# Kernel optimization log

Hardware: AMD Instinct MI355X
Metric: run time of the kernel (lower is better)

The kernel has to match this reference:

```python
import jax, jax.numpy as jnp
import numpy as np

B, S, D, H, L, FF, V, NB, G, C = 8, 1024, 256, 8, 2, 1024, 32000, 20000, 12, 4
DH = D // H


def _layer_norm(x, g, b, eps=1e-5):
    m = x.mean(-1, keepdims=True)
    v = ((x - m) ** 2).mean(-1, keepdims=True)
    return (x - m) / jnp.sqrt(v + eps) * g + b


def setup_inputs() -> dict:
    key = jax.random.key(0)
    ks = jax.random.split(key, 32)
    w = lambda k, shape, s=0.05: (jax.random.normal(k, shape, dtype=jnp.float32) * s)
    inp = {
        'input_ids': jax.random.randint(ks[0], (B, S), 0, V),
        'ngram_ids': jax.random.randint(ks[1], (V, G), 0, NB),
        'tfidf_scores': jax.random.uniform(ks[2], (V,), dtype=jnp.float32),
        'emb': jax.random.uniform(ks[3], (V, D), minval=-0.1, maxval=0.1, dtype=jnp.float32).at[0].set(0.0),  # padding_idx=0 row zeroed
        'pos_enc': jax.random.normal(ks[4], (1, S, D), dtype=jnp.float32) * 0.01,
        'bucket_emb': jax.random.uniform(ks[5], (NB, D), minval=-0.05, maxval=0.05, dtype=jnp.float32),
        'Wq': w(ks[6], (L, D, D)), 'bq': jnp.zeros((L, D)),
        'Wk': w(ks[7], (L, D, D)), 'bk': jnp.zeros((L, D)),
        'Wv': w(ks[8], (L, D, D)), 'bv': jnp.zeros((L, D)),
        'Wo': w(ks[9], (L, D, D)), 'bo': jnp.zeros((L, D)),
        'g1': jnp.ones((L, D)), 'be1': jnp.zeros((L, D)),
        'g2': jnp.ones((L, D)), 'be2': jnp.zeros((L, D)),
        'W1': w(ks[10], (L, D, FF)), 'b1': jnp.zeros((L, FF)),
        'W2': w(ks[11], (L, FF, D)), 'b2': jnp.zeros((L, D)),
        'alpha': jnp.full((L,), 0.1, dtype=jnp.float32),
        'gf': jnp.ones((D,)), 'bf': jnp.zeros((D,)),
        'Wc': jax.random.uniform(ks[12], (D, C), minval=-0.1, maxval=0.1, dtype=jnp.float32),
        'bc': jnp.zeros((C,)),
    }
    return inp


def reference(input_ids, ngram_ids, tfidf_scores, emb, pos_enc, bucket_emb,
              Wq, bq, Wk, bk, Wv, bv, Wo, bo, g1, be1, g2, be2,
              W1, b1, W2, b2, alpha, gf, bf, Wc, bc):
    pad_mask = input_ids == 0                      # (B,S) key padding mask
    x = emb[input_ids] + pos_enc[:, :S]            # (B,S,D)
    # char n-gram embedding: masked mean over n-gram buckets
    tok_ng = ngram_ids[jnp.clip(input_ids, 0, ngram_ids.shape[0] - 1)]   # (B,S,G)
    e_ng = bucket_emb[tok_ng]                       # (B,S,G,D)
    m = (tok_ng != 0)[..., None].astype(x.dtype)
    x = x + (e_ng * m).sum(axis=2) / jnp.clip(m.sum(axis=2), 1.0, None)
    # TF-IDF bias per key position
    bias_base = tfidf_scores[jnp.clip(input_ids, 0, tfidf_scores.shape[0] - 1)]  # (B,S)
    scale = DH ** -0.5
    for l in range(L):
        x2 = _layer_norm(x, g1[l], be1[l])
        Q = (x2 @ Wq[l] + bq[l]).reshape(B, S, H, DH).transpose(0, 2, 1, 3)
        K = (x2 @ Wk[l] + bk[l]).reshape(B, S, H, DH).transpose(0, 2, 1, 3)
        Vv = (x2 @ Wv[l] + bv[l]).reshape(B, S, H, DH).transpose(0, 2, 1, 3)
        scores = jnp.einsum('bhqd,bhkd->bhqk', Q, K) * scale
        scores = scores + (bias_base * alpha[l])[:, None, None, :]
        scores = jnp.where(pad_mask[:, None, None, :], -jnp.inf, scores)
        attn = jax.nn.softmax(scores, axis=-1)
        out = jnp.einsum('bhqk,bhkd->bhqd', attn, Vv).transpose(0, 2, 1, 3).reshape(B, S, D)
        x = x + (out @ Wo[l] + bo[l])
        x2 = _layer_norm(x, g2[l], be2[l])
        x = x + (jax.nn.relu(x2 @ W1[l] + b1[l]) @ W2[l] + b2[l])
    x = _layer_norm(x, gf, bf)
    return x[:, 0] @ Wc + bc                        # CLS pooling -> (B,4)
```

## Files before the change

### kernel.cpp

```cpp
#include <hip/hip_runtime.h>
#include <hip/hip_bf16.h>
#include <math.h>

#define TOK 8192
#define DIM 256
#define SEQ 1024
#define NH 8
#define FFD 1024
#define NL 2
#define VOCAB 32000
#define QKSTRIDE 2097152

typedef short bf16x8 __attribute__((ext_vector_type(8)));
typedef float f32x4 __attribute__((ext_vector_type(4)));

__device__ __forceinline__ ushort f2bf(float f) {
  union { float f; uint32_t u; } v; v.f = f;
  uint32_t r = v.u + 0x7FFFu + ((v.u >> 16) & 1u);
  return (ushort)(r >> 16);
}

__device__ __forceinline__ float bf2f(ushort u) {
  union { uint32_t u; float f; } v; v.u = (uint32_t)u << 16; return v.f;
}

__device__ __forceinline__ float exp2_n(float x) {
  float r; asm("v_exp_f32 %0, %1" : "=v"(r) : "v"(x)); return r;
}

__device__ __forceinline__ uint32_t cvtpk(float lo, float hi) {
  uint32_t r; asm("v_cvt_pk_bf16_f32 %0, %1, %2" : "=v"(r) : "v"(lo), "v"(hi));
  return r;
}

__device__ __forceinline__ void gload_lds16(const ushort* gp, ushort* lp) {
  __builtin_amdgcn_global_load_lds(
      (const __attribute__((address_space(1))) void*)gp,
      (__attribute__((address_space(3))) void*)lp, 16, 0, 0);
}

__global__ __launch_bounds__(256) void embed_ln_kernel(
    const int* __restrict__ ids, const int* __restrict__ ngram_ids,
    const float* __restrict__ tfidf, const float* __restrict__ emb,
    const float* __restrict__ pos, const float* __restrict__ bucket,
    const float* __restrict__ alpha, const float* __restrict__ g1,
    const float* __restrict__ be1,
    float* __restrict__ x, ushort* __restrict__ x2b, float* __restrict__ bm2)
{
  __shared__ int ngs[12];
  __shared__ float red[2][4];
  const int t = blockIdx.x;
  const int id = ids[t];
  int idc = id; if (idc < 0) idc = 0; if (idc > VOCAB-1) idc = VOCAB-1;
  if (threadIdx.x < 12) ngs[threadIdx.x] = ngram_ids[idc*12 + threadIdx.x];
  if (threadIdx.x == 0) {
    const float tf = tfidf[idc];
    const bool msk = (id == 0);
    const float l2e = 1.4426950408889634f;
    bm2[t]       = msk ? -1e30f : tf * alpha[0] * l2e;
    bm2[TOK + t] = msk ? -1e30f : tf * alpha[1] * l2e;
  }
  __syncthreads();
  const int d = threadIdx.x;
  const int s = t & (SEQ - 1);
  float v = emb[(size_t)id*DIM + d] + pos[s*DIM + d];
  float sum = 0.f; int cnt = 0;
  #pragma unroll
  for (int g = 0; g < 12; ++g) {
    const int ng = ngs[g];
    if (ng != 0) { sum += bucket[(size_t)ng*DIM + d]; cnt++; }
  }
  v += sum / fmaxf((float)cnt, 1.0f);
  x[(size_t)t*DIM + d] = v;
  const int wave = d >> 6, lane = d & 63;
  float sm = v;
  #pragma unroll
  for (int o = 32; o >= 1; o >>= 1) sm += __shfl_xor(sm, o);
  if (lane == 0) red[0][wave] = sm;
  __syncthreads();
  const float mean = (red[0][0]+red[0][1]+red[0][2]+red[0][3]) * (1.f/256.f);
  const float dv = v - mean;
  float q = dv * dv;
  #pragma unroll
  for (int o = 32; o >= 1; o >>= 1) q += __shfl_xor(q, o);
  if (lane == 0) red[1][wave] = q;
  __syncthreads();
  const float var = (red[1][0]+red[1][1]+red[1][2]+red[1][3]) * (1.f/256.f);
  const float rs = rsqrtf(var + 1e-5f);
  x2b[(size_t)t*DIM + d] = f2bf(dv*rs*g1[d] + be1[d]);
}

__global__ __launch_bounds__(256) void ln_bf16(
    const float* __restrict__ x, const float* __restrict__ g,
    const float* __restrict__ b, ushort* __restrict__ y)
{
  const int wave = threadIdx.x >> 6, lane = threadIdx.x & 63;
  const int row = blockIdx.x * 4 + wave;
  const float* xr = x + (size_t)row * DIM;
  float4 v = *reinterpret_cast<const float4*>(xr + lane*4);
  float s = v.x + v.y + v.z + v.w;
  #pragma unroll
  for (int o = 32; o >= 1; o >>= 1) s += __shfl_xor(s, o);
  const float mean = s * (1.f/256.f);
  const float dx0 = v.x-mean, dx1 = v.y-mean, dx2 = v.z-mean, dx3 = v.w-mean;
  float q = dx0*dx0 + dx1*dx1 + dx2*dx2 + dx3*dx3;
  #pragma unroll
  for (int o = 32; o >= 1; o >>= 1) q += __shfl_xor(q, o);
  const float rs = rsqrtf(q * (1.f/256.f) + 1e-5f);
  float4 gv = *reinterpret_cast<const float4*>(g + lane*4);
  float4 bv = *reinterpret_cast<const float4*>(b + lane*4);
  ushort4 o4;
  o4.x = f2bf(dx0*rs*gv.x + bv.x);
  o4.y = f2bf(dx1*rs*gv.y + bv.y);
  o4.z = f2bf(dx2*rs*gv.z + bv.z);
  o4.w = f2bf(dx3*rs*gv.w + bv.w);
  *reinterpret_cast<ushort4*>(y + (size_t)row*DIM + lane*4) = o4;
}

struct TDesc { const float* src; ushort* dst; int K; int N; };
struct TDescs { TDesc d[12]; };

__global__ __launch_bounds__(256) void transpose_conv(TDescs descs)
{
  const TDesc t = descs.d[blockIdx.z];
  const int k0 = blockIdx.x * 32, n0 = blockIdx.y * 32;
  if (k0 >= t.K || n0 >= t.N) return;
  __shared__ float tile[32][33];
  const int r = threadIdx.x >> 5, cc = threadIdx.x & 31;
  #pragma unroll
  for (int i = 0; i < 4; ++i)
    tile[r + i*8][cc] = t.src[(size_t)(k0 + r + i*8)*t.N + n0 + cc];
  __syncthreads();
  #pragma unroll
  for (int i = 0; i < 4; ++i)
    t.dst[(size_t)(n0 + r + i*8)*t.K + k0 + cc] = f2bf(tile[cc][r + i*8]);
}

template<int KDIM, int NDIM, int MODE>
__global__ __launch_bounds__(256) void gemm_mfma(
    const ushort* __restrict__ A, const ushort* __restrict__ Bw,
    const float* __restrict__ bias0, const float* __restrict__ bias1,
    const float* __restrict__ bias2, void* __restrict__ Cout,
    ushort* __restrict__ vtb)
{
  __shared__ ushort Al[3][64*32];
  __shared__ ushort Bl[3][128*32];
  const int bm = blockIdx.y * 64, bn = blockIdx.x * 128;
  const int tid = threadIdx.x, w = tid >> 6, lane = tid & 63;
  const int g = lane >> 4, c = lane & 15;
  const int lrow = lane >> 2, lc8 = (lane & 3) << 3;
  const f32x4 fzero = {0.f, 0.f, 0.f, 0.f};
  f32x4 acc[4][2];
  #pragma unroll
  for (int m = 0; m < 4; ++m) { acc[m][0] = fzero; acc[m][1] = fzero; }

#define STAGE(buf, k0)                                                         \
  {                                                                            \
    _Pragma("unroll")                                                          \
    for (int ch = w; ch < 12; ch += 4) {                                       \
      if (ch < 4)                                                              \
        gload_lds16(A + (size_t)(bm + ch*16 + lrow)*KDIM + (k0) + lc8,         \
                    &Al[buf][ch*512]);                                         \
      else                                                                     \
        gload_lds16(Bw + (size_t)(bn + (ch-4)*16 + lrow)*KDIM + (k0) + lc8,    \
                    &Bl[buf][(ch-4)*512]);                                     \
    }                                                                          \
  }

#define COMPUTE(buf)                                                           \
  {                                                                            \
    bf16x8 af[4], bfr[2];                                                      \
    _Pragma("unroll")                                                          \
    for (int m = 0; m < 4; ++m)                                                \
      af[m] = *(const bf16x8*)&Al[buf][(m*16 + c)*32 + g*8];                   \
    _Pragma("unroll")                                                          \
    for (int n = 0; n < 2; ++n)                                                \
      bfr[n] = *(const bf16x8*)&Bl[buf][(w*32 + n*16 + c)*32 + g*8];           \
    _Pragma("unroll")                                                          \
    for (int m = 0; m < 4; ++m)                                                \
      _Pragma("unroll")                                                        \
      for (int n = 0; n < 2; ++n)                                              \
        acc[m][n] = __builtin_amdgcn_mfma_f32_16x16x32_bf16(af[m], bfr[n], acc[m][n], 0, 0, 0); \
  }

  STAGE(0, 0);
  STAGE(1, 32);
  STAGE(2, 64);
  int buf = 0;
  for (int k0 = 0; k0 + 64 < KDIM; k0 += 32) {
    asm volatile("s_waitcnt vmcnt(6)" ::: "memory");
    __builtin_amdgcn_s_barrier();
    COMPUTE(buf);
    asm volatile("s_waitcnt lgkmcnt(0)" ::: "memory");
    __builtin_amdgcn_s_barrier();
    if (k0 + 96 < KDIM) STAGE(buf, k0 + 96);
    buf = (buf == 2) ? 0 : buf + 1;
  }
  asm volatile("s_waitcnt vmcnt(3)" ::: "memory");
  __builtin_amdgcn_s_barrier();
  COMPUTE(buf);
  buf = (buf == 2) ? 0 : buf + 1;
  asm volatile("s_waitcnt vmcnt(0)" ::: "memory");
  __builtin_amdgcn_s_barrier();
  COMPUTE(buf);
#undef STAGE
#undef COMPUTE

  #pragma unroll
  for (int m = 0; m < 4; ++m) {
    const int row0 = bm + m*16 + g*4;
    #pragma unroll
    for (int n = 0; n < 2; ++n) {
      const int col = bn + w*32 + n*16 + c;
      if (MODE == 1) {
        const float bb = bias0[col];
        #pragma unroll
        for (int r = 0; r < 4; ++r) {
          const float vv = fmaxf(acc[m][n][r] + bb, 0.f);
          const float other = __shfl_xor(vv, 1);
          if ((c & 1) == 0) {
            const uint32_t word = (uint32_t)f2bf(vv) | ((uint32_t)f2bf(other) << 16);
            *(uint32_t*)((ushort*)Cout + (size_t)(row0 + r)*NDIM + col) = word;
          }
        }
      } else if (MODE == 4) {
        const int b_ = row0 >> 10, s = row0 & (SEQ - 1);
        const int hd = col & 255;
        const int hh = hd >> 5, d = hd & 31;
        const float bb = (col < 256) ? bias0[hd] : bias1[hd];
        ushort* dst = ((col < 256) ? (ushort*)Cout : vtb)
                    + (((size_t)(b_*NH + hh)*SEQ + s) << 5) + d;
        #pragma unroll
        for (int r = 0; r < 4; ++r) {
          const float vv = acc[m][n][r] + bb;
          const float other = __shfl_xor(vv, 1);
          if ((c & 1) == 0) {
            const uint32_t word = (uint32_t)f2bf(vv) | ((uint32_t)f2bf(other) << 16);
            *(uint32_t*)(dst + (r << 5)) = word;
          }
        }
      } else {
        const int b_ = row0 >> 10, s = row0 & (SEQ - 1);
        if (col < 512) {
          const int hd = col & 255;
          const int hh = hd >> 5, d = hd & 31;
          const float bb = (col < 256) ? bias0[hd] : bias1[hd];
          ushort* dst = (ushort*)Cout + (col < 256 ? 0 : QKSTRIDE)
                      + (((size_t)(b_*NH + hh)*SEQ + s) << 5) + d;
          #pragma unroll
          for (int r = 0; r < 4; ++r) {
            const float vv = acc[m][n][r] + bb;
            const float other = __shfl_xor(vv, 1);
            if ((c & 1) == 0) {
              const uint32_t word = (uint32_t)f2bf(vv) | ((uint32_t)f2bf(other) << 16);
              *(uint32_t*)(dst + (r << 5)) = word;
            }
          }
        } else {
          const int hd = col - 512;
          const int hh = hd >> 5, d = hd & 31;
          const float bb = bias2[hd];
          const int sg = s >> 5, a = (s & 31) >> 2;
          const int pbase = (a & 3)*8 + (a >> 2)*4;
          ushort4 w4;
          w4.x = f2bf(acc[m][n][0] + bb);
          w4.y = f2bf(acc[m][n][1] + bb);
          w4.z = f2bf(acc[m][n][2] + bb);
          w4.w = f2bf(acc[m][n][3] + bb);
          *(ushort4*)(vtb + (((size_t)((b_*NH + hh)*32 + sg)*32 + d) << 5) + pbase) = w4;
        }
      }
    }
  }
}

template<int KDIM>
__global__ __launch_bounds__(256) void gemm64_acc(
    const ushort* __restrict__ A, const ushort* __restrict__ Bw,
    const float* __restrict__ bias, float* __restrict__ C)
{
  __shared__ ushort Al[3][64*32];
  __shared__ ushort Bl[3][64*32];
  const int bm = blockIdx.y * 64, bn = blockIdx.x * 64;
  const int tid = threadIdx.x, w = tid >> 6, lane = tid & 63;
  const int wm = w >> 1, wn = w & 1;
  const int g = lane >> 4, c = lane & 15;
  const int lrow = tid >> 2, lc8 = (tid & 3) << 3;
  const f32x4 fzero = {0.f, 0.f, 0.f, 0.f};
  f32x4 acc[2][2];
  acc[0][0] = fzero; acc[0][1] = fzero; acc[1][0] = fzero; acc[1][1] = fzero;

#define STAGE64(buf, k0)                                                       \
  {                                                                            \
    gload_lds16(A  + (size_t)(bm + lrow)*KDIM + (k0) + lc8,                    \
                &Al[buf][lrow*32 + lc8]);                                      \
    gload_lds16(Bw + (size_t)(bn + lrow)*KDIM + (k0) + lc8,                    \
                &Bl[buf][lrow*32 + lc8]);                                      \
  }

#define COMPUTE64(buf)                                                         \
  {                                                                            \
    bf16x8 af[2], bfr[2];                                                      \
    _Pragma("unroll")                                                          \
    for (int m = 0; m < 2; ++m)                                                \
      af[m] = *(const bf16x8*)&Al[buf][(wm*32 + m*16 + c)*32 + g*8];           \
    _Pragma("unroll")                                                          \
    for (int n = 0; n < 2; ++n)                                                \
      bfr[n] = *(const bf16x8*)&Bl[buf][(wn*32 + n*16 + c)*32 + g*8];          \
    _Pragma("unroll")                                                          \
    for (int m = 0; m < 2; ++m)                                                \
      _Pragma("unroll")                                                        \
      for (int n = 0; n < 2; ++n)                                              \
        acc[m][n] = __builtin_amdgcn_mfma_f32_16x16x32_bf16(af[m], bfr[n], acc[m][n], 0, 0, 0); \
  }

  STAGE64(0, 0);
  STAGE64(1, 32);
  STAGE64(2, 64);
  int buf = 0;
  for (int k0 = 0; k0 + 64 < KDIM; k0 += 32) {
    asm volatile("s_waitcnt vmcnt(4)" ::: "memory");
    __builtin_amdgcn_s_barrier();
    COMPUTE64(buf);
    asm volatile("s_waitcnt lgkmcnt(0)" ::: "memory");
    __builtin_amdgcn_s_barrier();
    if (k0 + 96 < KDIM) STAGE64(buf, k0 + 96);
    buf = (buf == 2) ? 0 : buf + 1;
  }
  asm volatile("s_waitcnt vmcnt(2)" ::: "memory");
  __builtin_amdgcn_s_barrier();
  COMPUTE64(buf);
  buf = (buf == 2) ? 0 : buf + 1;
  asm volatile("s_waitcnt vmcnt(0)" ::: "memory");
  __builtin_amdgcn_s_barrier();
  COMPUTE64(buf);
#undef STAGE64
#undef COMPUTE64

  #pragma unroll
  for (int m = 0; m < 2; ++m) {
    const int row0 = bm + wm*32 + m*16 + g*4;
    #pragma unroll
    for (int n = 0; n < 2; ++n) {
      const int col = bn + wn*32 + n*16 + c;
      const float bb = bias[col];
      #pragma unroll
      for (int r = 0; r < 4; ++r)
        C[(size_t)(row0 + r)*DIM + col] += acc[m][n][r] + bb;
    }
  }
}

__global__ __launch_bounds__(256) void attn_mfma(
    const ushort* __restrict__ qh, const ushort* __restrict__ kh,
    const ushort* __restrict__ vph, const float* __restrict__ bm2l,
    ushort* __restrict__ O)
{
  const int bid = blockIdx.x;
  const int lin = ((bid & 7) << 8) + (bid >> 3);
  const int tid = threadIdx.x, w = tid >> 6, lane = tid & 63;
  const int qw = lin & 31, h = (lin >> 5) & 7, b = lin >> 8;
  const int qb = qw << 5;
  const float scale2 = 0.17677669529663687f * 1.4426950408889634f;
  const int g = lane >> 4, c = lane & 15;
  const f32x4 fzero = {0.f, 0.f, 0.f, 0.f};
  const size_t bh = (size_t)(b*NH + h);

  const bf16x8 qf0 = *(const bf16x8*)(qh + ((bh*SEQ + qb + c)      << 5) + g*8);
  const bf16x8 qf1 = *(const bf16x8*)(qh + ((bh*SEQ + qb + 16 + c) << 5) + g*8);
  const ushort* kbase = kh  + ((bh*SEQ) << 5) + g*8;
  const ushort* vbase = vph + ((bh*SEQ) << 5) + g*8;
  const float*  bmb   = bm2l + b*SEQ;

  f32x4 oacc[2][2];
  oacc[0][0] = fzero; oacc[0][1] = fzero; oacc[1][0] = fzero; oacc[1][1] = fzero;
  float l0 = 0.f, l1 = 0.f;

  bf16x8 kfA[4], kfB[4];
  bf16x8 vfA[2][2], vfB[2][2];
  f32x4 bbA[4], bbB[4];

#define LOADT(kt, kf, vf, bb)                                                  \
  {                                                                            \
    _Pragma("unroll")                                                          \
    for (int ks = 0; ks < 4; ++ks) {                                           \
      kf[ks] = *(const bf16x8*)(kbase + (((kt) + ks*16 + c) << 5));            \
      bb[ks] = *(const f32x4*)(bmb + (kt) + ks*16 + g*4);                      \
    }                                                                          \
    _Pragma("unroll")                                                          \
    for (int ds_ = 0; ds_ < 2; ++ds_)                                          \
      _Pragma("unroll")                                                        \
      for (int sg = 0; sg < 2; ++sg)                                           \
        vf[ds_][sg] = *(const bf16x8*)(vbase +                                 \
            (((((kt) >> 5) + sg)*32 + ds_*16 + c) << 5));                      \
  }

#define ATILE(kf, vf, bb)                                                      \
  {                                                                            \
    f32x4 sf0[4], sf1[4];                                                      \
    __builtin_amdgcn_s_setprio(1);                                             \
    _Pragma("unroll")                                                          \
    for (int ks = 0; ks < 4; ++ks)                                             \
      sf0[ks] = __builtin_amdgcn_mfma_f32_16x16x32_bf16(kf[ks], qf0, fzero, 0, 0, 0); \
    _Pragma("unroll")                                                          \
    for (int ks = 0; ks < 4; ++ks)                                             \
      sf1[ks] = __builtin_amdgcn_mfma_f32_16x16x32_bf16(kf[ks], qf1, fzero, 0, 0, 0); \
    __builtin_amdgcn_s_setprio(0);                                             \
    float e0[4][4], e1[4][4];                                                  \
    _Pragma("unroll")                                                          \
    for (int ks = 0; ks < 4; ++ks)                                             \
      _Pragma("unroll")                                                        \
      for (int r = 0; r < 4; ++r) {                                            \
        e0[ks][r] = exp2_n(fmaf(sf0[ks][r], scale2, bb[ks][r]));               \
        e1[ks][r] = exp2_n(fmaf(sf1[ks][r], scale2, bb[ks][r]));               \
      }                                                                        \
    float a0 = 0.f, a1 = 0.f, a2 = 0.f, a3 = 0.f;                              \
    _Pragma("unroll")                                                          \
    for (int r = 0; r < 4; ++r) {                                              \
      a0 += e0[0][r] + e0[1][r]; a1 += e0[2][r] + e0[3][r];                    \
      a2 += e1[0][r] + e1[1][r]; a3 += e1[2][r] + e1[3][r];                    \
    }                                                                          \
    l0 += a0 + a1; l1 += a2 + a3;                                              \
    union { bf16x8 v; uint32_t u[4]; } p00, p01, p10, p11;                     \
    p00.u[0] = cvtpk(e0[0][0], e0[0][1]); p00.u[1] = cvtpk(e0[0][2], e0[0][3]);\
    p00.u[2] = cvtpk(e0[1][0], e0[1][1]); p00.u[3] = cvtpk(e0[1][2], e0[1][3]);\
    p01.u[0] = cvtpk(e0[2][0], e0[2][1]); p01.u[1] = cvtpk(e0[2][2], e0[2][3]);\
    p01.u[2] = cvtpk(e0[3][0], e0[3][1]); p01.u[3] = cvtpk(e0[3][2], e0[3][3]);\
    p10.u[0] = cvtpk(e1[0][0], e1[0][1]); p10.u[1] = cvtpk(e1[0][2], e1[0][3]);\
    p10.u[2] = cvtpk(e1[1][0], e1[1][1]); p10.u[3] = cvtpk(e1[1][2], e1[1][3]);\
    p11.u[0] = cvtpk(e1[2][0], e1[2][1]); p11.u[1] = cvtpk(e1[2][2], e1[2][3]);\
    p11.u[2] = cvtpk(e1[3][0], e1[3][1]); p11.u[3] = cvtpk(e1[3][2], e1[3][3]);\
    __builtin_amdgcn_s_setprio(1);                                             \
    oacc[0][0] = __builtin_amdgcn_mfma_f32_16x16x32_bf16(vf[0][0], p00.v, oacc[0][0], 0, 0, 0); \
    oacc[0][1] = __builtin_amdgcn_mfma_f32_16x16x32_bf16(vf[1][0], p00.v, oacc[0][1], 0, 0, 0); \
    oacc[1][0] = __builtin_amdgcn_mfma_f32_16x16x32_bf16(vf[0][0], p10.v, oacc[1][0], 0, 0, 0); \
    oacc[1][1] = __builtin_amdgcn_mfma_f32_16x16x32_bf16(vf[1][0], p10.v, oacc[1][1], 0, 0, 0); \
    oacc[0][0] = __builtin_amdgcn_mfma_f32_16x16x32_bf16(vf[0][1], p01.v, oacc[0][0], 0, 0, 0); \
    oacc[0][1] = __builtin_amdgcn_mfma_f32_16x16x32_bf16(vf[1][1], p01.v, oacc[0][1], 0, 0, 0); \
    oacc[1][0] = __builtin_amdgcn_mfma_f32_16x16x32_bf16(vf[0][1], p11.v, oacc[1][0], 0, 0, 0); \
    oacc[1][1] = __builtin_amdgcn_mfma_f32_16x16x32_bf16(vf[1][1], p11.v, oacc[1][1], 0, 0, 0); \
    __builtin_amdgcn_s_setprio(0);                                             \
  }

  const int kt0 = w << 8;
  LOADT(kt0, kfA, vfA, bbA);
  LOADT(kt0 + 64, kfB, vfB, bbB);
  ATILE(kfA, vfA, bbA);
  LOADT(kt0 + 128, kfA, vfA, bbA);
  ATILE(kfB, vfB, bbB);
  LOADT(kt0 + 192, kfB, vfB, bbB);
  ATILE(kfA, vfA, bbA);
  ATILE(kfB, vfB, bbB);
#undef LOADT
#undef ATILE

  __shared__ float Lo[4][64][19];
  #pragma unroll
  for (int q = 0; q < 2; ++q)
    #pragma unroll
    for (int ds_ = 0; ds_ < 2; ++ds_)
      #pragma unroll
      for (int i = 0; i < 4; ++i)
        Lo[w][lane][q*8 + ds_*4 + i] = oacc[q][ds_][i];
  Lo[w][lane][16] = l0;
  Lo[w][lane][17] = l1;
  __syncthreads();
  if (w < 2) {
    const int q = w;
    float o[8] = {0.f,0.f,0.f,0.f,0.f,0.f,0.f,0.f};
    float ls = 0.f;
    #pragma unroll
    for (int ww = 0; ww < 4; ++ww) {
      ls += Lo[ww][lane][16 + q];
      #pragma unroll
      for (int i = 0; i < 8; ++i) o[i] += Lo[ww][lane][q*8 + i];
    }
    ls += __shfl_xor(ls, 16);
    ls += __shfl_xor(ls, 32);
    const float inv = 1.f / ls;
    ushort* orow = O + (size_t)(b*SEQ + qb + q*16 + c)*DIM + h*32 + g*4;
    const uint32_t w0 = (uint32_t)f2bf(o[0]*inv) | ((uint32_t)f2bf(o[1]*inv) << 16);
    const uint32_t w1 = (uint32_t)f2bf(o[2]*inv) | ((uint32_t)f2bf(o[3]*inv) << 16);
    const uint32_t w2 = (uint32_t)f2bf(o[4]*inv) | ((uint32_t)f2bf(o[5]*inv) << 16);
    const uint32_t w3 = (uint32_t)f2bf(o[6]*inv) | ((uint32_t)f2bf(o[7]*inv) << 16);
    *(uint32_t*)(orow)      = w0;
    *(uint32_t*)(orow + 2)  = w1;
    *(uint32_t*)(orow + 16) = w2;
    *(uint32_t*)(orow + 18) = w3;
  }
}

__global__ __launch_bounds__(256) void q8_kernel(
    const ushort* __restrict__ x2b, const ushort* __restrict__ Wq1,
    const float* __restrict__ bq1, float* __restrict__ q8f)
{
  const int b = blockIdx.x, tid = threadIdx.x;
  __shared__ float xrow[256];
  xrow[tid] = bf2f(x2b[(size_t)(b*SEQ)*DIM + tid]);
  __syncthreads();
  const ushort* wrow = Wq1 + (size_t)tid*DIM;
  float acc = bq1[tid];
  #pragma unroll
  for (int k8 = 0; k8 < 32; ++k8) {
    const bf16x8 wv = *(const bf16x8*)(wrow + k8*8);
    #pragma unroll
    for (int j = 0; j < 8; ++j)
      acc = fmaf(bf2f((ushort)wv[j]), xrow[k8*8 + j], acc);
  }
  q8f[b*DIM + tid] = acc;
}

__global__ __launch_bounds__(256) void attn_decode(
    const float* __restrict__ q8f, const ushort* __restrict__ kh,
    const ushort* __restrict__ vh, const float* __restrict__ bm2l,
    float* __restrict__ obuf)
{
  const int b = blockIdx.x >> 3, h = blockIdx.x & 7;
  const int tid = threadIdx.x;
  const float scale2 = 0.17677669529663687f * 1.4426950408889634f;
  __shared__ float qv[32];
  if (tid < 32) qv[tid] = q8f[b*DIM + h*32 + tid];
  __syncthreads();
  const ushort* kb = kh + (((size_t)(b*NH + h))*SEQ << 5);
  const ushort* vb = vh + (((size_t)(b*NH + h))*SEQ << 5);
  const float* bias = bm2l + b*SEQ;
  float o[32];
  #pragma unroll
  for (int d = 0; d < 32; ++d) o[d] = 0.f;
  float lsum = 0.f;
  #pragma unroll
  for (int kk = 0; kk < 4; ++kk) {
    const int key = kk*256 + tid;
    const ushort* kr = kb + (key << 5);
    float dot = 0.f;
    #pragma unroll
    for (int i = 0; i < 4; ++i) {
      const bf16x8 kv8 = *(const bf16x8*)(kr + i*8);
      #pragma unroll
      for (int j = 0; j < 8; ++j)
        dot = fmaf(bf2f((ushort)kv8[j]), qv[i*8 + j], dot);
    }
    const float e = exp2_n(fmaf(dot, scale2, bias[key]));
    lsum += e;
    const ushort* vr = vb + (key << 5);
    #pragma unroll
    for (int i = 0; i < 4; ++i) {
      const bf16x8 vv8 = *(const bf16x8*)(vr + i*8);
      #pragma unroll
      for (int j = 0; j < 8; ++j)
        o[i*8 + j] = fmaf(e, bf2f((ushort)vv8[j]), o[i*8 + j]);
    }
  }
  __shared__ float red[256][33];
  #pragma unroll
  for (int d = 0; d < 32; ++d) red[tid][d] = o[d];
  red[tid][32] = lsum;
  __syncthreads();
  __shared__ float fin[33];
  if (tid < 33) {
    float s = 0.f;
    for (int t = 0; t < 256; ++t) s += red[t][tid];
    fin[tid] = s;
  }
  __syncthreads();
  if (tid < 32)
    obuf[b*DIM + h*32 + tid] = fin[tid] / fin[32];
}

__global__ __launch_bounds__(256) void tail_wo_ln(
    const float* __restrict__ obuf, const ushort* __restrict__ WoT1,
    const float* __restrict__ bo1, const float* __restrict__ g21,
    const float* __restrict__ be21, float* __restrict__ x,
    ushort* __restrict__ t2b)
{
  const int b = blockIdx.x, tid = threadIdx.x;
  const int wave = tid >> 6, lane = tid & 63;
  __shared__ float orow[256];
  __shared__ float red[2][4];
  orow[tid] = obuf[b*DIM + tid];
  __syncthreads();
  const ushort* wrow = WoT1 + (size_t)tid*DIM;
  float acc = bo1[tid];
  #pragma unroll
  for (int k8 = 0; k8 < 32; ++k8) {
    const bf16x8 wv = *(const bf16x8*)(wrow + k8*8);
    #pragma unroll
    for (int j = 0; j < 8; ++j)
      acc = fmaf(bf2f((ushort)wv[j]), orow[k8*8 + j], acc);
  }
  float* xp = x + (size_t)(b*SEQ)*DIM + tid;
  const float newx = *xp + acc;
  *xp = newx;
  float sm = newx;
  #pragma unroll
  for (int o = 32; o >= 1; o >>= 1) sm += __shfl_xor(sm, o);
  if (lane == 0) red[0][wave] = sm;
  __syncthreads();
  const float mean = (red[0][0]+red[0][1]+red[0][2]+red[0][3]) * (1.f/256.f);
  const float dv = newx - mean;
  float q = dv * dv;
  #pragma unroll
  for (int o = 32; o >= 1; o >>= 1) q += __shfl_xor(q, o);
  if (lane == 0) red[1][wave] = q;
  __syncthreads();
  const float var = (red[1][0]+red[1][1]+red[1][2]+red[1][3]) * (1.f/256.f);
  const float rs = rsqrtf(var + 1e-5f);
  t2b[b*DIM + tid] = f2bf(dv*rs*g21[tid] + be21[tid]);
}

__global__ __launch_bounds__(256) void tail_ff1(
    const ushort* __restrict__ t2b, const ushort* __restrict__ W1T1,
    const float* __restrict__ b11, ushort* __restrict__ midr)
{
  const int b = blockIdx.x >> 2, c4 = blockIdx.x & 3, tid = threadIdx.x;
  __shared__ float trow[256];
  trow[tid] = bf2f(t2b[b*DIM + tid]);
  __syncthreads();
  const int col = c4*256 + tid;
  const ushort* wrow = W1T1 + (size_t)col*DIM;
  float acc = b11[col];
  #pragma unroll
  for (int k8 = 0; k8 < 32; ++k8) {
    const bf16x8 wv = *(const bf16x8*)(wrow + k8*8);
    #pragma unroll
    for (int j = 0; j < 8; ++j)
      acc = fmaf(bf2f((ushort)wv[j]), trow[k8*8 + j], acc);
  }
  midr[b*FFD + col] = f2bf(fmaxf(acc, 0.f));
}

__global__ __launch_bounds__(256) void tail_ff2(
    const ushort* __restrict__ midr, const ushort* __restrict__ W2T1,
    const float* __restrict__ b21, float* __restrict__ x)
{
  const int b = blockIdx.x, tid = threadIdx.x;
  __shared__ float mrow[1024];
  #pragma unroll
  for (int i = 0; i < 4; ++i)
    mrow[i*256 + tid] = bf2f(midr[b*FFD + i*256 + tid]);
  __syncthreads();
  const ushort* wrow = W2T1 + (size_t)tid*FFD;
  float acc = b21[tid];
  #pragma unroll
  for (int k8 = 0; k8 < 128; ++k8) {
    const bf16x8 wv = *(const bf16x8*)(wrow + k8*8);
    #pragma unroll
    for (int j = 0; j < 8; ++j)
      acc = fmaf(bf2f((ushort)wv[j]), mrow[k8*8 + j], acc);
  }
  x[(size_t)(b*SEQ)*DIM + tid] += acc;
}

__global__ __launch_bounds__(256) void cls_kernel(
    const float* __restrict__ x, const float* __restrict__ gf,
    const float* __restrict__ bf, const float* __restrict__ Wc,
    const float* __restrict__ bc, float* __restrict__ out)
{
  const int b = blockIdx.x;
  const int tid = threadIdx.x;
  const int wave = tid >> 6, lane = tid & 63;
  const float* xr = x + (size_t)b * SEQ * DIM;
  const float v = xr[tid];
  __shared__ float redm[4], redv[4], redc[4][4];
  float s = v;
  #pragma unroll
  for (int o = 32; o >= 1; o >>= 1) s += __shfl_xor(s, o);
  if (lane == 0) redm[wave] = s;
  __syncthreads();
  const float mean = (redm[0]+redm[1]+redm[2]+redm[3]) * (1.f/256.f);
  const float dv = v - mean;
  float q = dv * dv;
  #pragma unroll
  for (int o = 32; o >= 1; o >>= 1) q += __shfl_xor(q, o);
  if (lane == 0) redv[wave] = q;
  __syncthreads();
  const float var = (redv[0]+redv[1]+redv[2]+redv[3]) * (1.f/256.f);
  const float rs = rsqrtf(var + 1e-5f);
  const float yn = dv*rs*gf[tid] + bf[tid];
  float pc[4];
  #pragma unroll
  for (int cc = 0; cc < 4; ++cc) pc[cc] = yn * Wc[tid*4 + cc];
  #pragma unroll
  for (int cc = 0; cc < 4; ++cc) {
    #pragma unroll
    for (int o = 32; o >= 1; o >>= 1) pc[cc] += __shfl_xor(pc[cc], o);
  }
  if (lane == 0) {
    #pragma unroll
    for (int cc = 0; cc < 4; ++cc) redc[wave][cc] = pc[cc];
  }
  __syncthreads();
  if (tid < 4)
    out[b*4 + tid] = redc[0][tid] + redc[1][tid] + redc[2][tid] + redc[3][tid] + bc[tid];
}

extern "C" void kernel_launch(void* const* d_in, const int* in_sizes, int n_in,
                              void* d_out, int out_size, void* d_ws, size_t ws_size,
                              hipStream_t stream)
{
  const int*   ids    = (const int*)d_in[0];
  const int*   ngrams = (const int*)d_in[1];
  const float* tfidf  = (const float*)d_in[2];
  const float* emb    = (const float*)d_in[3];
  const float* pos    = (const float*)d_in[4];
  const float* bucket = (const float*)d_in[5];
  const float* Wq = (const float*)d_in[6];  const float* bq = (const float*)d_in[7];
  const float* Wk = (const float*)d_in[8];  const float* bk = (const float*)d_in[9];
  const float* Wv = (const float*)d_in[10]; const float* bv = (const float*)d_in[11];
  const float* Wo = (const float*)d_in[12]; const float* bo = (const float*)d_in[13];
  const float* g1 = (const float*)d_in[14]; const float* be1= (const float*)d_in[15];
  const float* g2 = (const float*)d_in[16]; const float* be2= (const float*)d_in[17];
  const float* W1 = (const float*)d_in[18]; const float* b1 = (const float*)d_in[19];
  const float* W2 = (const float*)d_in[20]; const float* b2 = (const float*)d_in[21];
  const float* alpha = (const float*)d_in[22];
  const float* gf = (const float*)d_in[23]; const float* bf = (const float*)d_in[24];
  const float* Wc = (const float*)d_in[25]; const float* bc = (const float*)d_in[26];

  uint8_t* base = (uint8_t*)d_ws;
  float*  x      = (float*)  base;
  ushort* x2b    = (ushort*)(base + 8388608);
  ushort* qkh    = (ushort*)(base + 12582912);
  ushort* vtb    = (ushort*)(base + 20971520);
  ushort* attb   = (ushort*)(base + 25165824);
  ushort* midb   = (ushort*)(base + 29360128);
  float*  bm2    = (float*) (base + 46137344);
  ushort* WqkvT  = (ushort*)(base + 46202880);
  ushort* WoT    = (ushort*)(base + 46989312);
  ushort* W1T    = (ushort*)(base + 47251456);
  ushort* W2T    = (ushort*)(base + 48300032);

  float*  q8f  = (float*)attb;
  float*  obuf = (float*)(base + 25165824 + 8192);
  ushort* t2b  = (ushort*)(base + 25165824 + 16384);
  ushort* midr = (ushort*)(base + 25165824 + 20480);

  TDescs td;
  for (int l = 0; l < NL; ++l) {
    td.d[6*l+0] = { Wq + (size_t)l*DIM*DIM, WqkvT + (size_t)l*768*DIM +   0*DIM, DIM, DIM };
    td.d[6*l+1] = { Wk + (size_t)l*DIM*DIM, WqkvT + (size_t)l*768*DIM + 256*DIM, DIM, DIM };
    td.d[6*l+2] = { Wv + (size_t)l*DIM*DIM, WqkvT + (size_t)l*768*DIM + 512*DIM, DIM, DIM };
    td.d[6*l+3] = { Wo + (size_t)l*DIM*DIM, WoT  + (size_t)l*DIM*DIM,  DIM, DIM };
    td.d[6*l+4] = { W1 + (size_t)l*DIM*FFD, W1T  + (size_t)l*FFD*DIM,  DIM, FFD };
    td.d[6*l+5] = { W2 + (size_t)l*FFD*DIM, W2T  + (size_t)l*DIM*FFD,  FFD, DIM };
  }
  transpose_conv<<<dim3(32, 32, 12), 256, 0, stream>>>(td);

  embed_ln_kernel<<<TOK, 256, 0, stream>>>(
      ids, ngrams, tfidf, emb, pos, bucket, alpha, g1, be1, x, x2b, bm2);

  const dim3 gqkv(6, TOK/64), gkv(4, TOK/64), gff1(8, TOK/64), g64(4, TOK/64);

  gemm_mfma<256, 768, 3><<<gqkv, 256, 0, stream>>>(
      x2b, WqkvT, bq, bk, bv, qkh, vtb);
  attn_mfma<<<2048, 256, 0, stream>>>(qkh, qkh + QKSTRIDE, vtb, bm2, attb);
  gemm64_acc<256><<<g64, 256, 0, stream>>>(attb, WoT, bo, x);
  ln_bf16<<<TOK/4, 256, 0, stream>>>(x, g2, be2, x2b);
  gemm_mfma<256, 1024, 1><<<gff1, 256, 0, stream>>>(
      x2b, W1T, b1, nullptr, nullptr, midb, nullptr);
  gemm64_acc<1024><<<g64, 256, 0, stream>>>(midb, W2T, b2, x);

  ln_bf16<<<TOK/4, 256, 0, stream>>>(x, g1 + DIM, be1 + DIM, x2b);
  gemm_mfma<256, 512, 4><<<gkv, 256, 0, stream>>>(
      x2b, WqkvT + (size_t)768*DIM + 256*DIM, bk + DIM, bv + DIM, nullptr,
      qkh + QKSTRIDE, vtb);
  q8_kernel<<<8, 256, 0, stream>>>(x2b, WqkvT + (size_t)768*DIM, bq + DIM, q8f);
  attn_decode<<<64, 256, 0, stream>>>(q8f, qkh + QKSTRIDE, vtb, bm2 + TOK, obuf);
  tail_wo_ln<<<8, 256, 0, stream>>>(obuf, WoT + DIM*DIM, bo + DIM,
                                    g2 + DIM, be2 + DIM, x, t2b);
  tail_ff1<<<32, 256, 0, stream>>>(t2b, W1T + FFD*DIM, b1 + FFD, midr);
  tail_ff2<<<8, 256, 0, stream>>>(midr, W2T + DIM*FFD, b2 + DIM, x);

  cls_kernel<<<8, 256, 0, stream>>>(x, gf, bf, Wc, bc, (float*)d_out);
}
```

Baseline: 173.1 us.

## Fuse CLS-token decode tail kernels and fold Q projection into attention decode

Folds the per-head Q projection for the CLS token into the attention decode kernel. Each block computes its 32 Q values from the LN output row, which removes the separate q8 kernel. The Wo, LN2, FF1, FF2, final LN and classifier steps now run in one kernel per batch row, keeping intermediates in shared memory at fp32 instead of round-tripping bf16 buffers through global memory. This cuts five kernel launches and their dependency gaps. The cost is less parallelism in FF1, which goes from 32 blocks to 8, each doing four column passes serially.

```diff
diff --git a/kernel.cpp b/kernel.cpp
--- a/kernel.cpp
+++ b/kernel.cpp
@@ -490,36 +490,31 @@
   }
 }
 
-__global__ __launch_bounds__(256) void q8_kernel(
+__global__ __launch_bounds__(256) void attn_decode(
     const ushort* __restrict__ x2b, const ushort* __restrict__ Wq1,
-    const float* __restrict__ bq1, float* __restrict__ q8f)
-{
-  const int b = blockIdx.x, tid = threadIdx.x;
-  __shared__ float xrow[256];
-  xrow[tid] = bf2f(x2b[(size_t)(b*SEQ)*DIM + tid]);
-  __syncthreads();
-  const ushort* wrow = Wq1 + (size_t)tid*DIM;
-  float acc = bq1[tid];
-  #pragma unroll
-  for (int k8 = 0; k8 < 32; ++k8) {
-    const bf16x8 wv = *(const bf16x8*)(wrow + k8*8);
-    #pragma unroll
-    for (int j = 0; j < 8; ++j)
-      acc = fmaf(bf2f((ushort)wv[j]), xrow[k8*8 + j], acc);
-  }
-  q8f[b*DIM + tid] = acc;
-}
-
-__global__ __launch_bounds__(256) void attn_decode(
-    const float* __restrict__ q8f, const ushort* __restrict__ kh,
+    const float* __restrict__ bq1, const ushort* __restrict__ kh,
     const ushort* __restrict__ vh, const float* __restrict__ bm2l,
     float* __restrict__ obuf)
 {
   const int b = blockIdx.x >> 3, h = blockIdx.x & 7;
   const int tid = threadIdx.x;
   const float scale2 = 0.17677669529663687f * 1.4426950408889634f;
+  __shared__ float xrow[256];
   __shared__ float qv[32];
-  if (tid < 32) qv[tid] = q8f[b*DIM + h*32 + tid];
+  xrow[tid] = bf2f(x2b[(size_t)(b*SEQ)*DIM + tid]);
+  __syncthreads();
+  if (tid < 32) {
+    const ushort* wrow = Wq1 + (size_t)(h*32 + tid)*DIM;
+    float acc = bq1[h*32 + tid];
+    #pragma unroll
+    for (int k8 = 0; k8 < 32; ++k8) {
+      const bf16x8 wv = *(const bf16x8*)(wrow + k8*8);
+      #pragma unroll
+      for (int j = 0; j < 8; ++j)
+        acc = fmaf(bf2f((ushort)wv[j]), xrow[k8*8 + j], acc);
+    }
+    qv[tid] = acc;
+  }
   __syncthreads();
   const ushort* kb = kh + (((size_t)(b*NH + h))*SEQ << 5);
   const ushort* vb = vh + (((size_t)(b*NH + h))*SEQ << 5);
@@ -567,37 +562,90 @@
     obuf[b*DIM + h*32 + tid] = fin[tid] / fin[32];
 }
 
-__global__ __launch_bounds__(256) void tail_wo_ln(
+__global__ __launch_bounds__(256) void tail_fused(
     const float* __restrict__ obuf, const ushort* __restrict__ WoT1,
     const float* __restrict__ bo1, const float* __restrict__ g21,
-    const float* __restrict__ be21, float* __restrict__ x,
-    ushort* __restrict__ t2b)
+    const float* __restrict__ be21,
+    const ushort* __restrict__ W1T1, const float* __restrict__ b11,
+    const ushort* __restrict__ W2T1, const float* __restrict__ b21,
+    const float* __restrict__ x, const float* __restrict__ gf,
+    const float* __restrict__ bfb, const float* __restrict__ Wc,
+    const float* __restrict__ bc, float* __restrict__ out)
 {
   const int b = blockIdx.x, tid = threadIdx.x;
   const int wave = tid >> 6, lane = tid & 63;
   __shared__ float orow[256];
+  __shared__ float t2row[256];
+  __shared__ float mid[1024];
   __shared__ float red[2][4];
+  __shared__ float redc[4][4];
   orow[tid] = obuf[b*DIM + tid];
   __syncthreads();
-  const ushort* wrow = WoT1 + (size_t)tid*DIM;
-  float acc = bo1[tid];
-  #pragma unroll
-  for (int k8 = 0; k8 < 32; ++k8) {
-    const bf16x8 wv = *(const bf16x8*)(wrow + k8*8);
-    #pragma unroll
-    for (int j = 0; j < 8; ++j)
-      acc = fmaf(bf2f((ushort)wv[j]), orow[k8*8 + j], acc);
-  }
-  float* xp = x + (size_t)(b*SEQ)*DIM + tid;
-  const float newx = *xp + acc;
-  *xp = newx;
-  float sm = newx;
+  {
+    const ushort* wrow = WoT1 + (size_t)tid*DIM;
+    float acc = bo1[tid];
+    #pragma unroll
+    for (int k8 = 0; k8 < 32; ++k8) {
+      const bf16x8 wv = *(const bf16x8*)(wrow + k8*8);
+      #pragma unroll
+      for (int j = 0; j < 8; ++j)
+        acc = fmaf(bf2f((ushort)wv[j]), orow[k8*8 + j], acc);
+    }
+    const float newx = x[(size_t)(b*SEQ)*DIM + tid] + acc;
+    float sm = newx;
+    #pragma unroll
+    for (int o = 32; o >= 1; o >>= 1) sm += __shfl_xor(sm, o);
+    if (lane == 0) red[0][wave] = sm;
+    __syncthreads();
+    const float mean = (red[0][0]+red[0][1]+red[0][2]+red[0][3]) * (1.f/256.f);
+    const float dv = newx - mean;
+    float q = dv * dv;
+    #pragma unroll
+    for (int o = 32; o >= 1; o >>= 1) q += __shfl_xor(q, o);
+    if (lane == 0) red[1][wave] = q;
+    __syncthreads();
+    const float var = (red[1][0]+red[1][1]+red[1][2]+red[1][3]) * (1.f/256.f);
+    const float rs = rsqrtf(var + 1e-5f);
+    t2row[tid] = dv*rs*g21[tid] + be21[tid];
+    orow[tid] = newx;
+  }
+  __syncthreads();
+  #pragma unroll
+  for (int cc = 0; cc < 4; ++cc) {
+    const int col = cc*256 + tid;
+    const ushort* wrow = W1T1 + (size_t)col*DIM;
+    float acc = b11[col];
+    #pragma unroll
+    for (int k8 = 0; k8 < 32; ++k8) {
+      const bf16x8 wv = *(const bf16x8*)(wrow + k8*8);
+      #pragma unroll
+      for (int j = 0; j < 8; ++j)
+        acc = fmaf(bf2f((ushort)wv[j]), t2row[k8*8 + j], acc);
+    }
+    mid[col] = fmaxf(acc, 0.f);
+  }
+  __syncthreads();
+  float x2;
+  {
+    const ushort* wrow = W2T1 + (size_t)tid*FFD;
+    float acc = b21[tid];
+    #pragma unroll
+    for (int k8 = 0; k8 < 128; ++k8) {
+      const bf16x8 wv = *(const bf16x8*)(wrow + k8*8);
+      #pragma unroll
+      for (int j = 0; j < 8; ++j)
+        acc = fmaf(bf2f((ushort)wv[j]), mid[k8*8 + j], acc);
+    }
+    x2 = orow[tid] + acc;
+  }
+  __syncthreads();
+  float sm = x2;
   #pragma unroll
   for (int o = 32; o >= 1; o >>= 1) sm += __shfl_xor(sm, o);
   if (lane == 0) red[0][wave] = sm;
   __syncthreads();
   const float mean = (red[0][0]+red[0][1]+red[0][2]+red[0][3]) * (1.f/256.f);
-  const float dv = newx - mean;
+  const float dv = x2 - mean;
   float q = dv * dv;
   #pragma unroll
   for (int o = 32; o >= 1; o >>= 1) q += __shfl_xor(q, o);
@@ -605,78 +653,7 @@
   __syncthreads();
   const float var = (red[1][0]+red[1][1]+red[1][2]+red[1][3]) * (1.f/256.f);
   const float rs = rsqrtf(var + 1e-5f);
-  t2b[b*DIM + tid] = f2bf(dv*rs*g21[tid] + be21[tid]);
-}
-
-__global__ __launch_bounds__(256) void tail_ff1(
-    const ushort* __restrict__ t2b, const ushort* __restrict__ W1T1,
-    const float* __restrict__ b11, ushort* __restrict__ midr)
-{
-  const int b = blockIdx.x >> 2, c4 = blockIdx.x & 3, tid = threadIdx.x;
-  __shared__ float trow[256];
-  trow[tid] = bf2f(t2b[b*DIM + tid]);
-  __syncthreads();
-  const int col = c4*256 + tid;
-  const ushort* wrow = W1T1 + (size_t)col*DIM;
-  float acc = b11[col];
-  #pragma unroll
-  for (int k8 = 0; k8 < 32; ++k8) {
-    const bf16x8 wv = *(const bf16x8*)(wrow + k8*8);
-    #pragma unroll
-    for (int j = 0; j < 8; ++j)
-      acc = fmaf(bf2f((ushort)wv[j]), trow[k8*8 + j], acc);
-  }
-  midr[b*FFD + col] = f2bf(fmaxf(acc, 0.f));
-}
-
-__global__ __launch_bounds__(256) void tail_ff2(
-    const ushort* __restrict__ midr, const ushort* __restrict__ W2T1,
-    const float* __restrict__ b21, float* __restrict__ x)
-{
-  const int b = blockIdx.x, tid = threadIdx.x;
-  __shared__ float mrow[1024];
-  #pragma unroll
-  for (int i = 0; i < 4; ++i)
-    mrow[i*256 + tid] = bf2f(midr[b*FFD + i*256 + tid]);
-  __syncthreads();
-  const ushort* wrow = W2T1 + (size_t)tid*FFD;
-  float acc = b21[tid];
-  #pragma unroll
-  for (int k8 = 0; k8 < 128; ++k8) {
-    const bf16x8 wv = *(const bf16x8*)(wrow + k8*8);
-    #pragma unroll
-    for (int j = 0; j < 8; ++j)
-      acc = fmaf(bf2f((ushort)wv[j]), mrow[k8*8 + j], acc);
-  }
-  x[(size_t)(b*SEQ)*DIM + tid] += acc;
-}
-
-__global__ __launch_bounds__(256) void cls_kernel(
-    const float* __restrict__ x, const float* __restrict__ gf,
-    const float* __restrict__ bf, const float* __restrict__ Wc,
-    const float* __restrict__ bc, float* __restrict__ out)
-{
-  const int b = blockIdx.x;
-  const int tid = threadIdx.x;
-  const int wave = tid >> 6, lane = tid & 63;
-  const float* xr = x + (size_t)b * SEQ * DIM;
-  const float v = xr[tid];
-  __shared__ float redm[4], redv[4], redc[4][4];
-  float s = v;
-  #pragma unroll
-  for (int o = 32; o >= 1; o >>= 1) s += __shfl_xor(s, o);
-  if (lane == 0) redm[wave] = s;
-  __syncthreads();
-  const float mean = (redm[0]+redm[1]+redm[2]+redm[3]) * (1.f/256.f);
-  const float dv = v - mean;
-  float q = dv * dv;
-  #pragma unroll
-  for (int o = 32; o >= 1; o >>= 1) q += __shfl_xor(q, o);
-  if (lane == 0) redv[wave] = q;
-  __syncthreads();
-  const float var = (redv[0]+redv[1]+redv[2]+redv[3]) * (1.f/256.f);
-  const float rs = rsqrtf(var + 1e-5f);
-  const float yn = dv*rs*gf[tid] + bf[tid];
+  const float yn = dv*rs*gf[tid] + bfb[tid];
   float pc[4];
   #pragma unroll
   for (int cc = 0; cc < 4; ++cc) pc[cc] = yn * Wc[tid*4 + cc];
@@ -729,10 +706,7 @@
   ushort* W1T    = (ushort*)(base + 47251456);
   ushort* W2T    = (ushort*)(base + 48300032);
 
-  float*  q8f  = (float*)attb;
   float*  obuf = (float*)(base + 25165824 + 8192);
-  ushort* t2b  = (ushort*)(base + 25165824 + 16384);
-  ushort* midr = (ushort*)(base + 25165824 + 20480);
 
   TDescs td;
   for (int l = 0; l < NL; ++l) {
@@ -763,12 +737,11 @@
   gemm_mfma<256, 512, 4><<<gkv, 256, 0, stream>>>(
       x2b, WqkvT + (size_t)768*DIM + 256*DIM, bk + DIM, bv + DIM, nullptr,
       qkh + QKSTRIDE, vtb);
-  q8_kernel<<<8, 256, 0, stream>>>(x2b, WqkvT + (size_t)768*DIM, bq + DIM, q8f);
-  attn_decode<<<64, 256, 0, stream>>>(q8f, qkh + QKSTRIDE, vtb, bm2 + TOK, obuf);
-  tail_wo_ln<<<8, 256, 0, stream>>>(obuf, WoT + DIM*DIM, bo + DIM,
-                                    g2 + DIM, be2 + DIM, x, t2b);
-  tail_ff1<<<32, 256, 0, stream>>>(t2b, W1T + FFD*DIM, b1 + FFD, midr);
-  tail_ff2<<<8, 256, 0, stream>>>(midr, W2T + DIM*FFD, b2 + DIM, x);
-
-  cls_kernel<<<8, 256, 0, stream>>>(x, gf, bf, Wc, bc, (float*)d_out);
-}
+  attn_decode<<<64, 256, 0, stream>>>(
+      x2b, WqkvT + (size_t)768*DIM, bq + DIM,
+      qkh + QKSTRIDE, vtb, bm2 + TOK, obuf);
+  tail_fused<<<8, 256, 0, stream>>>(
+      obuf, WoT + DIM*DIM, bo + DIM, g2 + DIM, be2 + DIM,
+      W1T + FFD*DIM, b1 + FFD, W2T + DIM*FFD, b2 + DIM,
+      x, gf, bf, Wc, bc, (float*)d_out);
+}
```

Result: slower. 189.2 us (+9.3%).
